# Optimization experiments

Measured on AMD Instinct MI355X. Metric: run time of the kernel, lower is better.

## Reference

```python
import math
import jax, jax.numpy as jnp
import numpy as np

ROUNDS = 4
BUCKET_LEN = 64
NEG_BIG = -1e9
NEG_SELF = -1e5
EPS = 1e-12


def look_back(x):
    # x: [B, n_buckets, bucket_len, ...]; prepend previous bucket (circular) along bucket_len axis
    return jnp.concatenate([jnp.roll(x, 1, axis=1), x], axis=2)


def gather_dim1(x, idx):
    # torch expand_gather: broadcast x and idx to common shape, gather along axis 1
    shape = np.broadcast_shapes(x.shape, idx.shape)
    return jnp.take_along_axis(jnp.broadcast_to(x, shape), jnp.broadcast_to(idx, shape), axis=1)


def setup_inputs() -> dict:
    key = jax.random.key(0)
    k1, k2, k3 = jax.random.split(key, 3)
    B, L, d_k = 16, 4096, 64
    n_buckets = L // BUCKET_LEN
    query = jax.random.normal(k1, (B, L, d_k), dtype=jnp.float32)
    value = jax.random.normal(k2, (B, L, d_k), dtype=jnp.float32)
    rand_matrix = jax.random.normal(k3, (B, d_k, ROUNDS, n_buckets // 2), dtype=jnp.float32)
    return {"query": query, "value": value, "rand_matrix": rand_matrix, "seed": 0}


def lsh_hashes(query, rand_matrix):
    # LocalitySensitiveHash.forward
    B, L, d_k = query.shape
    qn = query / jnp.maximum(jnp.linalg.norm(query, axis=-1, keepdims=True), EPS)
    rm = rand_matrix / jnp.linalg.norm(rand_matrix, axis=1, keepdims=True)
    mm = jnp.einsum('bld,bdrn->blrn', qn, rm)  # [B, L, rounds, n_buckets//2]
    h = jnp.argmax(jnp.concatenate([mm, -mm], axis=-1), axis=-1).astype(jnp.int32)  # [B, L, rounds]
    return h * L + jnp.arange(L, dtype=jnp.int32)[None, :, None]  # unique per position


def _lsh_attention(query, value, rand_matrix):
    B, L, d_k = query.shape
    R, bl = ROUNDS, BUCKET_LEN
    nb = L // bl

    h = lsh_hashes(query, rand_matrix)
    sorted_hashes = jnp.sort(h, axis=1)
    hash_indice = jnp.argsort(h, axis=1)               # [B, L, R]
    original_indice = jnp.argsort(hash_indice, axis=1)  # reverse_sort

    # reorder queries by hash, bucketize: [B, nb, bl, d_k, R]
    rq = gather_dim1(query[:, :, :, None], hash_indice[:, :, None, :]).reshape(B, nb, bl, d_k, R)
    lb_key = look_back(rq)
    lb_key = lb_key / jnp.maximum(jnp.linalg.norm(lb_key, axis=-2, keepdims=True), EPS)
    scores = jnp.einsum('bnidr,bnjdr->bnijr', rq, lb_key) / math.sqrt(d_k)  # [B, nb, bl, 2bl, R]

    # mask: different buckets, causal, self
    sh = sorted_hashes.reshape(B, nb, bl, R) // L  # bucket id
    scores = jnp.where(sh[..., None, :] != look_back(sh)[..., None, :, :], NEG_BIG, scores)
    qi = hash_indice.reshape(B, nb, bl, R).astype(jnp.int32)
    ki = look_back(qi)  # [B, nb, 2bl, R]
    scores = jnp.where(qi[..., None, :] < ki[..., None, :, :], NEG_BIG, scores)
    scores = jnp.where(qi[..., None, :] == ki[..., None, :, :], NEG_SELF, scores)

    # duplicate-key counting across rounds (get_dup_keys)
    ki_full = jnp.broadcast_to(ki[:, :, None, :, :], (B, nb, bl, 2 * bl, R)).reshape(B, L, 2 * bl, R)
    ki_full = gather_dim1(ki_full, original_indice[:, :, None, :])
    flat = ki_full.reshape(B, L, 2 * bl * R)
    s_idx = jnp.argsort(flat, axis=-1)
    s = jnp.take_along_axis(flat, s_idx, axis=-1)
    counts = jnp.ones_like(s)
    for i in range(1, R):
        eq = (s[..., i:] == s[..., :-i]).astype(s.dtype)
        counts = counts + jnp.pad(eq, ((0, 0), (0, 0), (i, 0))) + jnp.pad(eq, ((0, 0), (0, 0), (0, i)))
    inv = jnp.argsort(s_idx, axis=-1)
    count_key = jnp.take_along_axis(counts, inv, axis=-1).reshape(B, L, 2 * bl, R)
    count_key = gather_dim1(count_key, hash_indice[:, :, None, :])

    # duplicate-adjusted softmax
    scores = scores.reshape(B, L, 2 * bl, R)
    lse = jax.nn.logsumexp(scores, axis=2)  # [B, L, R]
    softmax_qk = jnp.exp(scores - jnp.log(count_key.astype(scores.dtype)) - lse[:, :, None, :])

    rv = gather_dim1(value[:, :, :, None], hash_indice[:, :, None, :]).reshape(B, nb, bl, d_k, R)
    sm = softmax_qk.reshape(B, nb, bl, 2 * bl, R)
    attn = jnp.einsum('bnijr,bnjdr->bnidr', sm, look_back(rv)).reshape(B, L, d_k, R)
    attn = gather_dim1(attn, original_indice[:, :, None, :])
    lse = jnp.take_along_axis(lse, original_indice, axis=1)
    round_weights = jax.nn.softmax(lse, axis=1)  # dim=1 (length) exactly as in the source
    return jnp.einsum('bldr,blr->bld', attn, round_weights)


def reference(query, value, rand_matrix, seed):
    # seed is unused by the original forward body; dropout skipped (eval mode)
    return _lsh_attention(query, value, rand_matrix)
```

## Files before the change

kernel.cpp:

```cpp
#include <hip/hip_runtime.h>
#include <math.h>

#define B_  16
#define L_  4096
#define D_  64
#define R_  4
#define NB_ 64
#define BL_ 64
#define FIXCAP 8192

typedef _Float16 f16x8 __attribute__((ext_vector_type(8)));
typedef _Float16 f16x2 __attribute__((ext_vector_type(2)));
typedef float    f32x4 __attribute__((ext_vector_type(4)));


__global__ __launch_bounds__(64) void k_rmnorm(const float* __restrict__ rm,
                                               double* __restrict__ rmn,
                                               _Float16* __restrict__ rhi_g,
                                               _Float16* __restrict__ rlo_g,
                                               int* __restrict__ fix_cnt) {
    if (blockIdx.x == 0 && threadIdx.x == 0) *fix_cnt = 0;
    int blk = blockIdx.x;
    int b = blk >> 7, r = (blk >> 5) & 3, n = blk & 31;
    int d = threadIdx.x;
    double v = (double)rm[(((size_t)b * 64 + d) * 4 + r) * 32 + n];
    double sq = v * v;
    #pragma unroll
    for (int off = 32; off > 0; off >>= 1) sq += __shfl_down(sq, off);
    double tot = __shfl(sq, 0);
    double nv = v / sqrt(tot);
    rmn[(((size_t)b * 4 + r) * 32 + n) * 64 + d] = nv;
    float f = (float)nv;
    _Float16 hi = (_Float16)f;
    size_t gi = ((size_t)b * 128 + r * 32 + n) * 64 + d;
    rhi_g[gi] = hi;
    rlo_g[gi] = (_Float16)(f - (float)hi);
}

__global__ __launch_bounds__(256, 4) void k_hash(const float* __restrict__ q,
                                                 const float* __restrict__ value,
                                                 const _Float16* __restrict__ rhi_g,
                                                 const _Float16* __restrict__ rlo_g,
                                                 int* __restrict__ h_ws,
                                                 int* __restrict__ fix_cnt,
                                                 int* __restrict__ fix_list,
                                                 _Float16* __restrict__ qhf,
                                                 _Float16* __restrict__ khf,
                                                 _Float16* __restrict__ vhf) {
    __shared__ __align__(16) char smem[36864];
    _Float16* Rhi = (_Float16*)smem;
    _Float16* Rlo = (_Float16*)(smem + 18432);
    float*    Sc  = (float*)smem;

    int blk = blockIdx.x;
    int b = blk >> 6, chunk = blk & 63;
    int tid = threadIdx.x;
    int w = tid >> 6, lane = tid & 63, quad = lane >> 4, l15 = lane & 15;

    {
        int row = chunk * 64 + (tid >> 2), sub = tid & 3;
        const float4* vp = (const float4*)(value + ((size_t)(b * L_ + row)) * 64 + sub * 16);
        f16x8 h0, h1;
        #pragma unroll
        for (int c = 0; c < 2; c++) {
            float4 t0 = vp[2 * c], t1 = vp[2 * c + 1];
            f16x8& hd = c ? h1 : h0;
            hd[0]=(_Float16)t0.x; hd[1]=(_Float16)t0.y; hd[2]=(_Float16)t0.z; hd[3]=(_Float16)t0.w;
            hd[4]=(_Float16)t1.x; hd[5]=(_Float16)t1.y; hd[6]=(_Float16)t1.z; hd[7]=(_Float16)t1.w;
        }
        _Float16* dst = vhf + ((size_t)(b * L_ + row)) * 64 + sub * 16;
        *(f16x8*)dst = h0;
        *(f16x8*)(dst + 8) = h1;
    }

    {
        int row = tid >> 1, dh = (tid & 1) * 32;
        const _Float16* sh = rhi_g + ((size_t)b * 128 + row) * 64 + dh;
        const _Float16* sl = rlo_g + ((size_t)b * 128 + row) * 64 + dh;
        #pragma unroll
        for (int g = 0; g < 4; g++) {
            *(f16x8*)&Rhi[row * 72 + dh + g * 8] = *(const f16x8*)(sh + g * 8);
            *(f16x8*)&Rlo[row * 72 + dh + g * 8] = *(const f16x8*)(sl + g * 8);
        }
    }

    int qrow = chunk * 64 + w * 16 + l15;
    const float* qp = q + ((size_t)(b * L_ + qrow)) * 64;
    float qv[16];
    #pragma unroll
    for (int kt = 0; kt < 2; kt++) {
        float4 t0 = *(const float4*)(qp + kt * 32 + quad * 8);
        float4 t1 = *(const float4*)(qp + kt * 32 + quad * 8 + 4);
        qv[8*kt+0]=t0.x; qv[8*kt+1]=t0.y; qv[8*kt+2]=t0.z; qv[8*kt+3]=t0.w;
        qv[8*kt+4]=t1.x; qv[8*kt+5]=t1.y; qv[8*kt+6]=t1.z; qv[8*kt+7]=t1.w;
    }
    f16x8 Ahi[2], Alo[2];
    #pragma unroll
    for (int kt = 0; kt < 2; kt++) {
        #pragma unroll
        for (int j = 0; j < 8; j++) {
            _Float16 hi = (_Float16)qv[8*kt+j];
            Ahi[kt][j] = hi;
            Alo[kt][j] = (_Float16)(qv[8*kt+j] - (float)hi);
        }
    }
    {
        float ss = 0.f;
        #pragma unroll
        for (int j = 0; j < 16; j++) ss += qv[j] * qv[j];
        ss += __shfl_xor(ss, 16);
        ss += __shfl_xor(ss, 32);
        float nr = sqrtf(ss); if (nr < 1e-12f) nr = 1e-12f;
        float kscale = 0.18033688f / nr;
        _Float16* qd = qhf + ((size_t)(b * L_ + qrow)) * 64;
        _Float16* kd = khf + ((size_t)(b * L_ + qrow)) * 64;
        #pragma unroll
        for (int kt = 0; kt < 2; kt++) {
            *(f16x8*)(qd + kt * 32 + quad * 8) = Ahi[kt];
            f16x8 hv;
            #pragma unroll
            for (int j = 0; j < 8; j++) hv[j] = (_Float16)(qv[8*kt+j] * kscale);
            *(f16x8*)(kd + kt * 32 + quad * 8) = hv;
        }
    }
    __syncthreads();

    f32x4 acc[8];
    #pragma unroll
    for (int jt = 0; jt < 8; jt++) acc[jt] = (f32x4){0.f, 0.f, 0.f, 0.f};
    #pragma unroll
    for (int jt = 0; jt < 8; jt++) {
        #pragma unroll
        for (int kt = 0; kt < 2; kt++) {
            f16x8 bh = *(const f16x8*)&Rhi[(jt * 16 + l15) * 72 + kt * 32 + quad * 8];
            f16x8 bl = *(const f16x8*)&Rlo[(jt * 16 + l15) * 72 + kt * 32 + quad * 8];
            acc[jt] = __builtin_amdgcn_mfma_f32_16x16x32_f16(Ahi[kt], bh, acc[jt], 0, 0, 0);
            acc[jt] = __builtin_amdgcn_mfma_f32_16x16x32_f16(Ahi[kt], bl, acc[jt], 0, 0, 0);
            acc[jt] = __builtin_amdgcn_mfma_f32_16x16x32_f16(Alo[kt], bh, acc[jt], 0, 0, 0);
        }
    }
    __syncthreads();

    #pragma unroll
    for (int jt = 0; jt < 8; jt++) {
        #pragma unroll
        for (int reg = 0; reg < 4; reg++)
            Sc[(w * 16 + quad * 4 + reg) * 133 + jt * 16 + l15] = acc[jt][reg];
    }
    __syncthreads();

    {
        int row = tid & 63, r = tid >> 6;
        const float* sp = &Sc[row * 133 + r * 32];
        float v1 = -1e30f, v2 = -1e30f; int i1 = 0;
        #pragma unroll
        for (int n = 0; n < 32; n++) {
            float v = sp[n];
            float a = fabsf(v);
            int cand = n | ((__float_as_uint(v) >> 26) & 32);
            if (a > v1) i1 = cand;
            v2 = __builtin_amdgcn_fmed3f(a, v1, v2);
            v1 = fmaxf(a, v1);
        }
        int l = chunk * 64 + row;
        h_ws[((size_t)(b * 4 + r)) * L_ + l] = i1;
        if (v1 - v2 < 4e-5f) {
            int slot = atomicAdd(fix_cnt, 1);
            if (slot < FIXCAP) fix_list[slot] = (b << 14) | (r << 12) | l;
        }
    }
}

__global__ __launch_bounds__(64) void k_fix(const float* __restrict__ q,
                                            const double* __restrict__ rmn,
                                            const int* __restrict__ fix_cnt,
                                            const int* __restrict__ fix_list,
                                            int* __restrict__ h_ws) {
    int cnt = *fix_cnt; if (cnt > FIXCAP) cnt = FIXCAP;
    int lane = threadIdx.x;
    for (int i = blockIdx.x; i < cnt; i += gridDim.x) {
        int e = fix_list[i];
        int b = e >> 14, r = (e >> 12) & 3, l = e & 4095;
        int n = lane & 31;
        const double* rp = rmn + ((size_t)(b * 4 + r)) * 2048 + n * 64;
        const float* qr = q + ((size_t)(b * L_ + l)) * 64;
        double a0 = 0.0, a1 = 0.0, a2 = 0.0, a3 = 0.0;
        #pragma unroll
        for (int d = 0; d < 64; d += 4) {
            a0 += (double)qr[d]   * rp[d];
            a1 += (double)qr[d+1] * rp[d+1];
            a2 += (double)qr[d+2] * rp[d+2];
            a3 += (double)qr[d+3] * rp[d+3];
        }
        double acc = ((a0 + a1) + (a2 + a3));
        double v = (lane < 32) ? acc : -acc;
        int idx = lane;
        #pragma unroll
        for (int off = 1; off < 64; off <<= 1) {
            double ov = __shfl_xor(v, off);
            int   oidx = __shfl_xor(idx, off);
            if (ov > v || (ov == v && oidx < idx)) { v = ov; idx = oidx; }
        }
        if (lane == 0) h_ws[((size_t)(b * 4 + r)) * L_ + l] = idx;
    }
}

__global__ __launch_bounds__(256) void k_sort(const int* __restrict__ h_ws,
                                              int* __restrict__ hi_ws,
                                              int* __restrict__ oi_ws) {
    __shared__ __align__(16) unsigned short cnt[64 * 257];
    __shared__ __align__(16) unsigned short oi_s[256 * 17];
    __shared__ __align__(16) unsigned short hi_s[4096];
    __shared__ int part[256];

    int br = blockIdx.x;
    int t = threadIdx.x;
    const int* hp = h_ws + (size_t)br * L_;

    unsigned int* cz = (unsigned int*)cnt;
    #pragma unroll
    for (int i = 0; i < 33; i++) {
        int idx = i * 256 + t;
        if (idx < 8224) cz[idx] = 0;
    }

    int key[16];
    const int4* hp4 = (const int4*)(hp + t * 16);
    #pragma unroll
    for (int g = 0; g < 4; g++) {
        int4 v = hp4[g];
        key[g*4+0] = v.x; key[g*4+1] = v.y; key[g*4+2] = v.z; key[g*4+3] = v.w;
    }
    __syncthreads();

    #pragma unroll
    for (int k = 0; k < 16; k++) {
        unsigned short* c = &cnt[key[k] * 257 + t];
        *c = (unsigned short)(*c + 1);
    }
    __syncthreads();

    int u = t & 63, s = t >> 6;
    {
        int run = 0;
        int base_idx = u * 257 + s * 64;
        #pragma unroll 16
        for (int i = 0; i < 64; i++) {
            int c = cnt[base_idx + i];
            cnt[base_idx + i] = (unsigned short)run;
            run += c;
        }
        part[s * 64 + u] = run;
    }
    __syncthreads();

    if (t < 64) {
        int p0 = part[t], p1 = part[64 + t], p2 = part[128 + t], p3 = part[192 + t];
        int tot = p0 + p1 + p2 + p3;
        int v = tot;
        #pragma unroll
        for (int off = 1; off < 64; off <<= 1) {
            int o = __shfl_up(v, off);
            if (t >= off) v += o;
        }
        int base = v - tot;
        part[t]       = base;
        part[64 + t]  = base + p0;
        part[128 + t] = base + p0 + p1;
        part[192 + t] = base + p0 + p1 + p2;
    }
    __syncthreads();

    int sbase = s * 64;
    #pragma unroll
    for (int k = 0; k < 16; k++) {
        int uk = key[k];
        unsigned short* c = &cnt[uk * 257 + t];
        int pos = part[sbase + uk] + *c;
        *c = (unsigned short)(*c + 1);
        int idx = t * 16 + k;
        oi_s[(idx >> 4) * 17 + (idx & 15)] = (unsigned short)pos;
        hi_s[pos] = (unsigned short)idx;
    }
    __syncthreads();

    int* op  = oi_ws + (size_t)br * L_;
    int* hp2 = hi_ws + (size_t)br * L_;
    #pragma unroll
    for (int k = 0; k < 16; k++) {
        int e = k * 256 + t;
        op[e]  = (int)oi_s[(e >> 4) * 17 + (e & 15)];
        hp2[e] = (int)hi_s[e];
    }
}

__global__ __launch_bounds__(256) void k_meta(const int* __restrict__ h_ws,
                                              const int* __restrict__ hi_ws,
                                              const int* __restrict__ oi_ws,
                                              int4* __restrict__ meta_ws) {
    int gid = blockIdx.x * 256 + threadIdx.x;
    int br = gid >> 12, spos = gid & 4095;
    int b = br >> 2;
    int p = hi_ws[(size_t)br * L_ + spos];
    int hh = h_ws[(size_t)br * L_ + p];
    int pack = 0, packm1 = 0;
    #pragma unroll
    for (int r2 = 0; r2 < 4; r2++) {
        int bk = oi_ws[((size_t)(b * 4 + r2)) * L_ + p] >> 6;
        pack   |= bk << (8 * r2);
        packm1 |= ((bk + 63) & 63) << (8 * r2);
    }
    meta_ws[(size_t)br * L_ + spos] = make_int4(hh, p, pack, packm1);
}

__global__ __launch_bounds__(256, 4) void k_attn(const _Float16* __restrict__ qhf,
                                                 const _Float16* __restrict__ khf,
                                                 const _Float16* __restrict__ vhf,
                                                 const int4* __restrict__ meta_ws,
                                                 float* __restrict__ lse_ws,
                                                 _Float16* __restrict__ attn_ws) {
    __shared__ _Float16 Ksh[128 * 72];
    __shared__ _Float16 Vt[64 * 136];
    __shared__ int4 kmeta[128];

    int xcd = blockIdx.x & 7, slot = blockIdx.x >> 3;
    int b = xcd * 2 + (slot >> 8);
    int rem = slot & 255, n = rem >> 2, r = rem & 3;
    int tid = threadIdx.x;
    int w = tid >> 6, lane = tid & 63, quad = lane >> 4, l15 = lane & 15;
    int hibase = (b * 4 + r) * L_;
    const int4* mp = meta_ws + hibase;
    int nprev = (n + 63) & 63;

    {
        int j = tid >> 1, dh = (tid & 1) * 32;
        int spos = (j < 64) ? (nprev * 64 + j) : (n * 64 + (j - 64));
        int4 me = mp[spos];
        if (dh == 0) kmeta[j] = me;
        const _Float16* src = khf + ((size_t)(b * L_ + me.y)) * 64 + dh;
        #pragma unroll
        for (int g = 0; g < 4; g++)
            *(f16x8*)&Ksh[j * 72 + dh + g * 8] = *(const f16x8*)(src + g * 8);
    }
    __syncthreads();

    {
        int m = tid >> 2, sub = tid & 3;
        int y0 = kmeta[2 * m].y, y1 = kmeta[2 * m + 1].y;
        const _Float16* v0 = vhf + ((size_t)(b * L_ + y0)) * 64 + sub * 16;
        const _Float16* v1 = vhf + ((size_t)(b * L_ + y1)) * 64 + sub * 16;
        f16x8 a00 = *(const f16x8*)v0, a01 = *(const f16x8*)(v0 + 8);
        f16x8 a10 = *(const f16x8*)v1, a11 = *(const f16x8*)(v1 + 8);
        #pragma unroll
        for (int d = 0; d < 8; d++) {
            f16x2 hv = { a00[d], a10[d] };
            *(f16x2*)&Vt[(sub * 16 + d) * 136 + 2 * m] = hv;
            f16x2 hw = { a01[d], a11[d] };
            *(f16x2*)&Vt[(sub * 16 + 8 + d) * 136 + 2 * m] = hw;
        }
    }

    int qy = kmeta[64 + w * 16 + l15].y;
    const _Float16* qp = qhf + ((size_t)(b * L_ + qy)) * 64;
    f16x8 afr[2];
    afr[0] = *(const f16x8*)(qp + quad * 8);
    afr[1] = *(const f16x8*)(qp + 32 + quad * 8);

    f32x4 acc[8];
    #pragma unroll
    for (int jt = 0; jt < 8; jt++) acc[jt] = (f32x4){0.f, 0.f, 0.f, 0.f};
    __builtin_amdgcn_s_setprio(1);
    #pragma unroll
    for (int jt = 0; jt < 8; jt++) {
        #pragma unroll
        for (int kt = 0; kt < 2; kt++) {
            f16x8 bfr = *(const f16x8*)&Ksh[(jt * 16 + l15) * 72 + kt * 32 + quad * 8];
            acc[jt] = __builtin_amdgcn_mfma_f32_16x16x32_f16(afr[kt], bfr, acc[jt], 0, 0, 0);
        }
    }
    __builtin_amdgcn_s_setprio(0);

    int4 qm4[4], km4[8];
    #pragma unroll
    for (int reg = 0; reg < 4; reg++) qm4[reg] = kmeta[64 + w * 16 + quad * 4 + reg];
    #pragma unroll
    for (int jt = 0; jt < 8; jt++) km4[jt] = kmeta[jt * 16 + l15];
    __syncthreads();

    _Float16* Ph = Ksh;
    float lse_r[4], inv_r[4];
    #pragma unroll
    for (int reg = 0; reg < 4; reg++) {
        float s[8];
        #pragma unroll
        for (int jt = 0; jt < 8; jt++) {
            float v = acc[jt][reg];
            if (km4[jt].x != qm4[reg].x) v = -1.4426951e9f;
            if (qm4[reg].y < km4[jt].y)  v = -1.4426951e9f;
            if (qm4[reg].y == km4[jt].y) v = -144269.50f;
            s[jt] = v;
        }
        float m = s[0];
        #pragma unroll
        for (int jt = 1; jt < 8; jt++) m = fmaxf(m, s[jt]);
        #pragma unroll
        for (int off = 1; off < 16; off <<= 1) m = fmaxf(m, __shfl_xor(m, off));
        float te[8], sum = 0.f;
        #pragma unroll
        for (int jt = 0; jt < 8; jt++) { te[jt] = __builtin_amdgcn_exp2f(s[jt] - m); sum += te[jt]; }
        #pragma unroll
        for (int off = 1; off < 16; off <<= 1) sum += __shfl_xor(sum, off);
        inv_r[reg] = __builtin_amdgcn_rcpf(sum);
        lse_r[reg] = m * 0.6931472f + __logf(sum);
        int i = w * 16 + quad * 4 + reg;
        #pragma unroll
        for (int jt = 0; jt < 8; jt++) {
            int z1 = km4[jt].z ^ qm4[reg].z;
            int z2 = km4[jt].z ^ qm4[reg].w;
            int nz = __popc((z1 + 0x7f7f7f7f) & 0x80808080)
                   + __popc((z2 + 0x7f7f7f7f) & 0x80808080);
            float p = te[jt] * __builtin_amdgcn_rcpf((float)(8 - nz));
            Ph[i * 136 + jt * 16 + l15] = (_Float16)p;
        }
    }
    if (l15 == 0) {
        #pragma unroll
        for (int reg = 0; reg < 4; reg++)
            lse_ws[hibase + qm4[reg].y] = lse_r[reg];
    }
    __syncthreads();

    f32x4 oacc[4];
    #pragma unroll
    for (int nt = 0; nt < 4; nt++) oacc[nt] = (f32x4){0.f, 0.f, 0.f, 0.f};
    __builtin_amdgcn_s_setprio(1);
    #pragma unroll
    for (int kt = 0; kt < 4; kt++) {
        f16x8 pa = *(const f16x8*)&Ph[(w * 16 + l15) * 136 + kt * 32 + quad * 8];
        #pragma unroll
        for (int nt = 0; nt < 4; nt++) {
            f16x8 vb = *(const f16x8*)&Vt[(nt * 16 + l15) * 136 + kt * 32 + quad * 8];
            oacc[nt] = __builtin_amdgcn_mfma_f32_16x16x32_f16(pa, vb, oacc[nt], 0, 0, 0);
        }
    }
    __builtin_amdgcn_s_setprio(0);
    __syncthreads();

    _Float16* Pout = Ksh;
    #pragma unroll
    for (int nt = 0; nt < 4; nt++) {
        #pragma unroll
        for (int reg = 0; reg < 4; reg++) {
            int i = w * 16 + quad * 4 + reg;
            Pout[i * 72 + nt * 16 + l15] = (_Float16)(oacc[nt][reg] * inv_r[reg]);
        }
    }
    __syncthreads();

    {
        int row = tid >> 2, part = tid & 3;
        int y = kmeta[64 + row].y;
        _Float16* dst = attn_ws + ((size_t)hibase + y) * 64;
        f16x8 v0 = *(const f16x8*)&Pout[row * 72 + part * 8];
        f16x8 v1 = *(const f16x8*)&Pout[row * 72 + 32 + part * 8];
        *(f16x8*)(dst + part * 8) = v0;
        *(f16x8*)(dst + 32 + part * 8) = v1;
    }
}

__global__ __launch_bounds__(256) void k_rw(const float* __restrict__ lse_ws,
                                            float* __restrict__ rwmax,
                                            float* __restrict__ rwsum) {
    __shared__ float  red[256];
    __shared__ double redd[256];
    int br = blockIdx.x;
    const float* lp = lse_ws + (size_t)br * L_;
    int t = threadIdx.x;
    float m = -1e30f;
    for (int k = t; k < L_; k += 256) m = fmaxf(m, lp[k]);
    red[t] = m; __syncthreads();
    for (int s2 = 128; s2 > 0; s2 >>= 1) {
        if (t < s2) red[t] = fmaxf(red[t], red[t + s2]);
        __syncthreads();
    }
    float mm = red[0];
    double s = 0.0;
    for (int k = t; k < L_; k += 256) s += (double)expf(lp[k] - mm);
    redd[t] = s; __syncthreads();
    for (int s2 = 128; s2 > 0; s2 >>= 1) {
        if (t < s2) redd[t] += redd[t + s2];
        __syncthreads();
    }
    if (t == 0) { rwmax[br] = mm; rwsum[br] = (float)redd[0]; }
}

__global__ __launch_bounds__(256) void k_out(const _Float16* __restrict__ attn_ws,
                                             const float* __restrict__ lse_ws,
                                             const float* __restrict__ rwmax,
                                             const float* __restrict__ rwsum,
                                             float* __restrict__ out) {
    int gid = blockIdx.x * 256 + threadIdx.x;
    int g = gid & 7;
    size_t row = (size_t)(gid >> 3);
    int b = (int)(row >> 12), l = (int)(row & 4095);
    float o[8];
    #pragma unroll
    for (int k = 0; k < 8; k++) o[k] = 0.f;
    #pragma unroll
    for (int r = 0; r < 4; r++) {
        int br = b * 4 + r;
        float wgt = __expf(lse_ws[(size_t)br * L_ + l] - rwmax[br])
                  * __builtin_amdgcn_rcpf(rwsum[br]);
        f16x8 av = *(const f16x8*)&attn_ws[(((size_t)br * L_ + l) << 6) + g * 8];
        #pragma unroll
        for (int k = 0; k < 8; k++) o[k] += (float)av[k] * wgt;
    }
    float4* op = (float4*)(out + row * 64 + g * 8);
    op[0] = make_float4(o[0], o[1], o[2], o[3]);
    op[1] = make_float4(o[4], o[5], o[6], o[7]);
}

extern "C" void kernel_launch(void* const* d_in, const int* in_sizes, int n_in,
                              void* d_out, int out_size, void* d_ws, size_t ws_size,
                              hipStream_t stream) {
    const float* query = (const float*)d_in[0];
    const float* value = (const float*)d_in[1];
    const float* rm    = (const float*)d_in[2];
    char* ws = (char*)d_ws;
    double*    rmn    = (double*)ws;
    int*       h_ws   = (int*)(ws + ((size_t)1 << 20));
    int*       hi_ws  = (int*)(ws + ((size_t)2 << 20));
    int*       oi_ws  = (int*)(ws + ((size_t)3 << 20));
    float*     lse_ws = (float*)(ws + ((size_t)4 << 20));
    float*     rwmax  = (float*)(ws + ((size_t)5 << 20));
    float*     rwsum  = (float*)(ws + ((size_t)5 << 20) + 256);
    int*       fix_cnt= (int*)(ws + ((size_t)5 << 20) + 512);
    int*       fix_list=(int*)(ws + ((size_t)5 << 20) + 1024);
    _Float16*  attn_ws= (_Float16*)(ws + ((size_t)6 << 20));
    _Float16*  rhi_g  = (_Float16*)(ws + ((size_t)40 << 20));
    _Float16*  rlo_g  = (_Float16*)(ws + ((size_t)40 << 20) + ((size_t)1 << 19));
    int4*      meta_ws= (int4*)(ws + ((size_t)41 << 20));
    _Float16*  qhf    = (_Float16*)(ws + ((size_t)45 << 20));
    _Float16*  khf    = (_Float16*)(ws + ((size_t)53 << 20));
    _Float16*  vhf    = (_Float16*)(ws + ((size_t)61 << 20));
    float*     out    = (float*)d_out;

    hipLaunchKernelGGL(k_rmnorm, dim3(2048), dim3(64),  0, stream, rm, rmn, rhi_g, rlo_g, fix_cnt);
    hipLaunchKernelGGL(k_hash,   dim3(1024), dim3(256), 0, stream, query, value, rhi_g, rlo_g,
                       h_ws, fix_cnt, fix_list, qhf, khf, vhf);
    hipLaunchKernelGGL(k_fix,    dim3(64),   dim3(64),  0, stream, query, rmn,
                       fix_cnt, fix_list, h_ws);
    hipLaunchKernelGGL(k_sort,   dim3(64),   dim3(256), 0, stream, h_ws, hi_ws, oi_ws);
    hipLaunchKernelGGL(k_meta,   dim3(1024), dim3(256), 0, stream, h_ws, hi_ws, oi_ws, meta_ws);
    hipLaunchKernelGGL(k_attn,   dim3(4096), dim3(256), 0, stream,
                       qhf, khf, vhf, meta_ws, lse_ws, attn_ws);
    hipLaunchKernelGGL(k_rw,     dim3(64),   dim3(256), 0, stream, lse_ws, rwmax, rwsum);
    hipLaunchKernelGGL(k_out,    dim3(2048), dim3(256), 0, stream,
                       attn_ws, lse_ws, rwmax, rwsum, out);
}
```

Before: 162.9 us.

## Drop hash-index array; use bucket start offsets for range-based masking

The sort kernel stops writing the sorted-to-original index array and instead emits per-hash bucket start offsets. The meta kernel scatters each position's metadata to its sorted slot, storing the bucket start in place of the hash. The attention kernel then replaces the per-key hash and causal comparisons with a single unsigned range check against the bucket start, and loads only the z field of key metadata. This cuts global writes in the sort, reduces register and shared-memory loads for masking, and simplifies the mask arithmetic. The price is scattered writes in the meta kernel and a reliance on equal-hash keys being contiguous and in position order within the sorted sequence.

After: 160.4 us. About the same (-1.5%).

```diff
diff --git a/kernel.cpp b/kernel.cpp
--- a/kernel.cpp
+++ b/kernel.cpp
@@ -206,11 +206,10 @@
 }
 
 __global__ __launch_bounds__(256) void k_sort(const int* __restrict__ h_ws,
-                                              int* __restrict__ hi_ws,
-                                              int* __restrict__ oi_ws) {
+                                              int* __restrict__ oi_ws,
+                                              int* __restrict__ bstart_g) {
     __shared__ __align__(16) unsigned short cnt[64 * 257];
     __shared__ __align__(16) unsigned short oi_s[256 * 17];
-    __shared__ __align__(16) unsigned short hi_s[4096];
     __shared__ int part[256];
 
     int br = blockIdx.x;
@@ -264,6 +263,7 @@
             if (t >= off) v += o;
         }
         int base = v - tot;
+        bstart_g[br * 64 + t] = base;
         part[t]       = base;
         part[64 + t]  = base + p0;
         part[128 + t] = base + p0 + p1;
@@ -280,37 +280,36 @@
         *c = (unsigned short)(*c + 1);
         int idx = t * 16 + k;
         oi_s[(idx >> 4) * 17 + (idx & 15)] = (unsigned short)pos;
-        hi_s[pos] = (unsigned short)idx;
-    }
-    __syncthreads();
-
-    int* op  = oi_ws + (size_t)br * L_;
-    int* hp2 = hi_ws + (size_t)br * L_;
+    }
+    __syncthreads();
+
+    int* op = oi_ws + (size_t)br * L_;
     #pragma unroll
     for (int k = 0; k < 16; k++) {
         int e = k * 256 + t;
-        op[e]  = (int)oi_s[(e >> 4) * 17 + (e & 15)];
-        hp2[e] = (int)hi_s[e];
+        op[e] = (int)oi_s[(e >> 4) * 17 + (e & 15)];
     }
 }
 
 __global__ __launch_bounds__(256) void k_meta(const int* __restrict__ h_ws,
-                                              const int* __restrict__ hi_ws,
                                               const int* __restrict__ oi_ws,
+                                              const int* __restrict__ bstart_g,
                                               int4* __restrict__ meta_ws) {
     int gid = blockIdx.x * 256 + threadIdx.x;
-    int br = gid >> 12, spos = gid & 4095;
-    int b = br >> 2;
-    int p = hi_ws[(size_t)br * L_ + spos];
+    int br = gid >> 12, p = gid & 4095;
+    int b = br >> 2, rme = br & 3;
     int hh = h_ws[(size_t)br * L_ + p];
-    int pack = 0, packm1 = 0;
+    int pack = 0, packm1 = 0, mypos = 0;
     #pragma unroll
     for (int r2 = 0; r2 < 4; r2++) {
-        int bk = oi_ws[((size_t)(b * 4 + r2)) * L_ + p] >> 6;
+        int o = oi_ws[((size_t)(b * 4 + r2)) * L_ + p];
+        if (r2 == rme) mypos = o;
+        int bk = o >> 6;
         pack   |= bk << (8 * r2);
         packm1 |= ((bk + 63) & 63) << (8 * r2);
     }
-    meta_ws[(size_t)br * L_ + spos] = make_int4(hh, p, pack, packm1);
+    int sb = bstart_g[br * 64 + hh];
+    meta_ws[(size_t)br * L_ + mypos] = make_int4(sb, p, pack, packm1);
 }
 
 __global__ __launch_bounds__(256, 4) void k_attn(const _Float16* __restrict__ qhf,
@@ -380,24 +379,27 @@
     }
     __builtin_amdgcn_s_setprio(0);
 
-    int4 qm4[4], km4[8];
+    int4 qm4[4]; int km4z[8];
     #pragma unroll
     for (int reg = 0; reg < 4; reg++) qm4[reg] = kmeta[64 + w * 16 + quad * 4 + reg];
     #pragma unroll
-    for (int jt = 0; jt < 8; jt++) km4[jt] = kmeta[jt * 16 + l15];
+    for (int jt = 0; jt < 8; jt++) km4z[jt] = kmeta[jt * 16 + l15].z;
     __syncthreads();
 
     _Float16* Ph = Ksh;
     float lse_r[4], inv_r[4];
     #pragma unroll
     for (int reg = 0; reg < 4; reg++) {
+        int lo = qm4[reg].x - (n - 1) * 64;
+        int width = w * 16 + quad * 4 + reg + 64 - lo;
+        int jl = l15 - lo;
         float s[8];
         #pragma unroll
         for (int jt = 0; jt < 8; jt++) {
             float v = acc[jt][reg];
-            if (km4[jt].x != qm4[reg].x) v = -1.4426951e9f;
-            if (qm4[reg].y < km4[jt].y)  v = -1.4426951e9f;
-            if (qm4[reg].y == km4[jt].y) v = -144269.50f;
+            int ju = jt * 16 + jl;
+            v = ((unsigned)ju < (unsigned)width) ? v : -1.4426951e9f;
+            if (ju == width) v = -144269.50f;
             s[jt] = v;
         }
         float m = s[0];
@@ -415,8 +417,8 @@
         int i = w * 16 + quad * 4 + reg;
         #pragma unroll
         for (int jt = 0; jt < 8; jt++) {
-            int z1 = km4[jt].z ^ qm4[reg].z;
-            int z2 = km4[jt].z ^ qm4[reg].w;
+            int z1 = km4z[jt] ^ qm4[reg].z;
+            int z2 = km4z[jt] ^ qm4[reg].w;
             int nz = __popc((z1 + 0x7f7f7f7f) & 0x80808080)
                    + __popc((z2 + 0x7f7f7f7f) & 0x80808080);
             float p = te[jt] * __builtin_amdgcn_rcpf((float)(8 - nz));
@@ -529,13 +531,13 @@
     char* ws = (char*)d_ws;
     double*    rmn    = (double*)ws;
     int*       h_ws   = (int*)(ws + ((size_t)1 << 20));
-    int*       hi_ws  = (int*)(ws + ((size_t)2 << 20));
     int*       oi_ws  = (int*)(ws + ((size_t)3 << 20));
     float*     lse_ws = (float*)(ws + ((size_t)4 << 20));
     float*     rwmax  = (float*)(ws + ((size_t)5 << 20));
     float*     rwsum  = (float*)(ws + ((size_t)5 << 20) + 256);
     int*       fix_cnt= (int*)(ws + ((size_t)5 << 20) + 512);
     int*       fix_list=(int*)(ws + ((size_t)5 << 20) + 1024);
+    int*       bstart = (int*)(ws + ((size_t)5 << 20) + ((size_t)256 << 10));
     _Float16*  attn_ws= (_Float16*)(ws + ((size_t)6 << 20));
     _Float16*  rhi_g  = (_Float16*)(ws + ((size_t)40 << 20));
     _Float16*  rlo_g  = (_Float16*)(ws + ((size_t)40 << 20) + ((size_t)1 << 19));
@@ -550,8 +552,8 @@
                        h_ws, fix_cnt, fix_list, qhf, khf, vhf);
     hipLaunchKernelGGL(k_fix,    dim3(64),   dim3(64),  0, stream, query, rmn,
                        fix_cnt, fix_list, h_ws);
-    hipLaunchKernelGGL(k_sort,   dim3(64),   dim3(256), 0, stream, h_ws, hi_ws, oi_ws);
-    hipLaunchKernelGGL(k_meta,   dim3(1024), dim3(256), 0, stream, h_ws, hi_ws, oi_ws, meta_ws);
+    hipLaunchKernelGGL(k_sort,   dim3(64),   dim3(256), 0, stream, h_ws, oi_ws, bstart);
+    hipLaunchKernelGGL(k_meta,   dim3(1024), dim3(256), 0, stream, h_ws, oi_ws, bstart, meta_ws);
     hipLaunchKernelGGL(k_attn,   dim3(4096), dim3(256), 0, stream,
                        qhf, khf, vhf, meta_ws, lse_ws, attn_ws);
     hipLaunchKernelGGL(k_rw,     dim3(64),   dim3(256), 0, stream, lse_ws, rwmax, rwsum);
```
